# Optimization experiments

Measured on AMD Instinct MI355X. Metric: run time of the kernel, lower is better.

The kernel has to match this reference:

```python
import jax, jax.numpy as jnp
import numpy as np

N_NODES = 10000
N_EDGES = 320000
D = 128      # node/edge feature dim
H = 512      # MLP hidden width


def _mlp(x, W1, b1, W2, b2):
    return jax.nn.relu(x @ W1 + b1) @ W2 + b2


def setup_inputs() -> dict:
    key = jax.random.key(0)
    ks = jax.random.split(key, 8)
    s = lambda fan_in: 1.0 / np.sqrt(fan_in)
    return {
        "x": jax.random.normal(ks[0], (N_NODES, D), jnp.float32),
        "edge_index": jax.random.randint(ks[1], (2, N_EDGES), 0, N_NODES, jnp.int64),
        "edge_attr": jax.random.normal(ks[2], (N_EDGES, D), jnp.float32),
        "We1": jax.random.normal(ks[3], (3 * D, H), jnp.float32) * s(3 * D),
        "be1": jnp.zeros((H,), jnp.float32),
        "We2": jax.random.normal(ks[4], (H, D), jnp.float32) * s(H),
        "be2": jnp.zeros((D,), jnp.float32),
        "Wn1": jax.random.normal(ks[5], (2 * D, H), jnp.float32) * s(2 * D),
        "bn1": jnp.zeros((H,), jnp.float32),
        "Wn2": jax.random.normal(ks[6], (H, D), jnp.float32) * s(H),
        "bn2": jnp.zeros((D,), jnp.float32),
    }


def reference(x, edge_index, edge_attr, We1, be1, We2, be2, Wn1, bn1, Wn2, bn2):
    senders = edge_index[0]
    receivers = edge_index[1]
    # gather -> edge MLP
    edge_inputs = jnp.concatenate([x[senders], x[receivers], edge_attr], axis=-1)  # [E, 3D]
    updated_edge_attr = _mlp(edge_inputs, We1, be1, We2, be2)                      # [E, D]
    # scatter-add into receiving nodes
    aggregated = jax.ops.segment_sum(updated_edge_attr, receivers, num_segments=x.shape[0])  # [N, D]
    # node MLP
    node_inputs = jnp.concatenate([x, aggregated], axis=-1)                        # [N, 2D]
    updated_nodes = _mlp(node_inputs, Wn1, bn1, Wn2, bn2)                          # [N, D]
    return updated_nodes, updated_edge_attr
```

## Files before the change

### kernel.cpp

```cpp
#include <hip/hip_runtime.h>
#include <hip/hip_bf16.h>

#define N_NODES 10000
#define N_EDGES 320000
#define D 128
#define H 512

typedef __bf16 bf16x8 __attribute__((ext_vector_type(8)));
typedef float f32x4 __attribute__((ext_vector_type(4)));
typedef unsigned short u16x8 __attribute__((ext_vector_type(8)));

__device__ __forceinline__ unsigned short f2bf(float f) {
    union { float f; unsigned u; } v; v.f = f;
    unsigned r = v.u + 0x7fffu + ((v.u >> 16) & 1u);
    return (unsigned short)(r >> 16);
}

__global__ void cast_x_kernel(const float* __restrict__ x, unsigned short* __restrict__ xb) {
    int t = blockIdx.x * 256 + threadIdx.x;
    float4 v = reinterpret_cast<const float4*>(x)[t];
    ushort4 o;
    o.x = f2bf(v.x); o.y = f2bf(v.y); o.z = f2bf(v.z); o.w = f2bf(v.w);
    reinterpret_cast<ushort4*>(xb)[t] = o;
}

__global__ void swizzle_w_kernel(const float* __restrict__ W, unsigned short* __restrict__ out,
                                 int K, int Nn) {
    int t = blockIdx.x * 256 + threadIdx.x;
    int total = (K >> 5) * (Nn >> 4) * 64;
    if (t >= total) return;
    int lane = t & 63;
    int tile = t >> 6;
    int ntiles = Nn >> 4;
    int nt = tile % ntiles;
    int kt = tile / ntiles;
    int k0 = kt * 32 + (lane >> 4) * 8;
    int n  = nt * 16 + (lane & 15);
    unsigned short tmp[8];
#pragma unroll
    for (int j = 0; j < 8; ++j) tmp[j] = f2bf(W[(size_t)(k0 + j) * Nn + n]);
    ushort4* dst = reinterpret_cast<ushort4*>(out + (size_t)t * 8);
    dst[0] = *reinterpret_cast<ushort4*>(&tmp[0]);
    dst[1] = *reinterpret_cast<ushort4*>(&tmp[4]);
}

__global__ void hist_kernel(const int* __restrict__ eidx, int* __restrict__ deg) {
    int e = blockIdx.x * 256 + threadIdx.x;
    if (e < N_EDGES) atomicAdd(&deg[eidx[N_EDGES + e]], 1);
}

__global__ __launch_bounds__(1024) void scan_kernel(const int* __restrict__ deg,
                                                    int* __restrict__ rowstart,
                                                    int* __restrict__ cursor) {
    __shared__ int wsums[16];
    const int t = threadIdx.x;
    const int lane = t & 63, wv = t >> 6;
    const int base = t * 10;
    int loc[10];
    int s = 0;
#pragma unroll
    for (int i = 0; i < 10; ++i) {
        int v = (base + i < N_NODES) ? deg[base + i] : 0;
        loc[i] = s; s += v;
    }
    const int tot = s;
    int inc = tot;
#pragma unroll
    for (int d = 1; d < 64; d <<= 1) {
        int n = __shfl_up(inc, d, 64);
        if (lane >= d) inc += n;
    }
    if (lane == 63) wsums[wv] = inc;
    __syncthreads();
    if (t == 0) {
        int run = 0;
#pragma unroll
        for (int w = 0; w < 16; ++w) { int v = wsums[w]; wsums[w] = run; run += v; }
    }
    __syncthreads();
    const int off = wsums[wv] + inc - tot;
#pragma unroll
    for (int i = 0; i < 10; ++i) {
        int idx = base + i;
        if (idx < N_NODES) { int v = off + loc[i]; rowstart[idx] = v; cursor[idx] = v; }
    }
    if (t == 1023) rowstart[N_NODES] = off + tot;
}

__global__ void scatter_kernel(const int* __restrict__ eidx, int* __restrict__ cursor,
                               int* __restrict__ elist) {
    int e = blockIdx.x * 256 + threadIdx.x;
    if (e < N_EDGES) {
        int p = atomicAdd(&cursor[eidx[N_EDGES + e]], 1);
        elist[p] = e;
    }
}

__global__ __launch_bounds__(256) void agg_kernel(
    const float* __restrict__ out_edges,
    const int* __restrict__ rowstart,
    const int* __restrict__ elist,
    unsigned short* __restrict__ aggb)
{
    int node = blockIdx.x * 4 + (threadIdx.x >> 6);
    int lane = threadIdx.x & 63;
    int r0 = rowstart[node], r1 = rowstart[node + 1];
    float sx = 0.f, sy = 0.f;
    for (int j = r0; j < r1; ++j) {
        int e = elist[j];
        float2 v = *reinterpret_cast<const float2*>(&out_edges[(size_t)e * 128 + lane * 2]);
        sx += v.x; sy += v.y;
    }
    ushort2 o; o.x = f2bf(sx); o.y = f2bf(sy);
    *reinterpret_cast<ushort2*>(&aggb[(size_t)node * 128 + lane * 2]) = o;
}

__device__ __forceinline__ void gld_lds16(const void* g, void* l) {
    __builtin_amdgcn_global_load_lds((const __attribute__((address_space(1))) void*)g,
                                     (__attribute__((address_space(3))) void*)l, 16, 0, 0);
}

__device__ __forceinline__ void stage_a(int kt, unsigned short* Abuf, int wave, int lane,
                                        const unsigned short* aS, const unsigned short* aR,
                                        const float* aE) {
    if (kt < 8) {
        const unsigned short* src = (kt < 4) ? (aS + kt * 32) : (aR + (kt - 4) * 32);
        gld_lds16(src, Abuf + wave * 512);
    } else {
        const float* s = aE + (kt - 8) * 32;
        float4 v0 = *reinterpret_cast<const float4*>(s);
        float4 v1 = *reinterpret_cast<const float4*>(s + 4);
        u16x8 o;
        o[0] = f2bf(v0.x); o[1] = f2bf(v0.y); o[2] = f2bf(v0.z); o[3] = f2bf(v0.w);
        o[4] = f2bf(v1.x); o[5] = f2bf(v1.y); o[6] = f2bf(v1.z); o[7] = f2bf(v1.w);
        *reinterpret_cast<u16x8*>(Abuf + wave * 512 + lane * 8) = o;
    }
}

__device__ __forceinline__ void stage_b(int kt, unsigned short* Bbuf, int wave, int lane,
                                        const unsigned short* We1s) {
#pragma unroll
    for (int i = 0; i < 4; ++i) {
        int c = wave * 4 + i;
        const unsigned short* src = We1s + ((size_t)kt * 32 + c) * 512 + lane * 8;
        gld_lds16(src, Bbuf + c * 512);
    }
}

__global__ __launch_bounds__(512, 2) void edge_mlp_kernel(
    const unsigned short* __restrict__ xb,
    const int* __restrict__ eidx,
    const float* __restrict__ edge_attr,
    const unsigned short* __restrict__ We1s,
    const float* __restrict__ be1,
    const unsigned short* __restrict__ We2s,
    const float* __restrict__ be2,
    float* __restrict__ out_edges)
{
    __shared__ unsigned short smem[40960];
    unsigned short* const A0  = smem;
    unsigned short* const A1  = smem + 4096;
    unsigned short* const B0  = smem + 8192;
    unsigned short* const B1  = smem + 24576;
    unsigned short* const sH0 = smem + 4096;
    unsigned short* const sH1 = smem + 21504;

    const int tid = threadIdx.x;
    const int wave = tid >> 6, lane = tid & 63;
    const int wr = wave >> 2, wc = wave & 3;
    const int l15 = lane & 15;
    const int Q = lane >> 4;
    const int e0 = blockIdx.x * 128;

    const int rs = wave * 16 + (lane >> 2);
    const int sq = (lane & 3) ^ (rs & 3);
    const int nS = eidx[e0 + rs];
    const int nR = eidx[N_EDGES + e0 + rs];
    const unsigned short* aS = xb + (size_t)nS * 128 + sq * 8;
    const unsigned short* aR = xb + (size_t)nR * 128 + sq * 8;
    const float*          aE = edge_attr + (size_t)(e0 + rs) * 128 + sq * 8;

    f32x4 acc1[8][4];
#pragma unroll
    for (int j = 0; j < 8; ++j)
#pragma unroll
        for (int mt = 0; mt < 4; ++mt) acc1[j][mt] = (f32x4){0.f, 0.f, 0.f, 0.f};
    f32x4 acc2[2][4];
#pragma unroll
    for (int nn = 0; nn < 2; ++nn)
#pragma unroll
        for (int mt = 0; mt < 4; ++mt) acc2[nn][mt] = (f32x4){0.f, 0.f, 0.f, 0.f};

    stage_a(0, A0, wave, lane, aS, aR, aE);
    stage_b(0, B0, wave, lane, We1s);
    __syncthreads();

#pragma unroll
    for (int kt = 0; kt < 12; ++kt) {
        unsigned short* const Ac = (kt & 1) ? A1 : A0;
        unsigned short* const Bc = (kt & 1) ? B1 : B0;
        if (kt < 11) {
            stage_a(kt + 1, (kt & 1) ? A0 : A1, wave, lane, aS, aR, aE);
            stage_b(kt + 1, (kt & 1) ? B0 : B1, wave, lane, We1s);
        }
        bf16x8 a[4];
#pragma unroll
        for (int mt = 0; mt < 4; ++mt) {
            int R = wr * 64 + mt * 16 + l15;
            a[mt] = *reinterpret_cast<const bf16x8*>(&Ac[R * 32 + ((Q ^ (R & 3)) * 8)]);
        }
#pragma unroll
        for (int j = 0; j < 8; ++j) {
            int ntile = (j >> 1) * 8 + wc * 2 + (j & 1);
            bf16x8 b = *reinterpret_cast<const bf16x8*>(&Bc[ntile * 512 + lane * 8]);
#pragma unroll
            for (int mt = 0; mt < 4; ++mt)
                acc1[j][mt] = __builtin_amdgcn_mfma_f32_16x16x32_bf16(a[mt], b, acc1[j][mt], 0, 0, 0);
        }
        __syncthreads();
    }

#define EWRITE_H(hh, dst)                                                     \
    {                                                                         \
        _Pragma("unroll")                                                     \
        for (int nn = 0; nn < 2; ++nn) {                                      \
            int cc = (wc * 2 + nn) * 16 + l15;                                \
            float bias = be1[(hh) * 128 + cc];                                \
            _Pragma("unroll")                                                 \
            for (int mt = 0; mt < 4; ++mt)                                    \
                _Pragma("unroll")                                             \
                for (int r = 0; r < 4; ++r) {                                 \
                    float v = acc1[(hh) * 2 + nn][mt][r] + bias;              \
                    v = v > 0.f ? v : 0.f;                                    \
                    int row = wr * 64 + mt * 16 + (lane >> 4) * 4 + r;        \
                    (dst)[row * 136 + cc] = f2bf(v);                          \
                }                                                             \
        }                                                                     \
    }

    EWRITE_H(0, sH0);
    __syncthreads();
#pragma unroll
    for (int h = 0; h < 4; ++h) {
        unsigned short* const cur = (h & 1) ? sH1 : sH0;
        unsigned short* const nxt = (h & 1) ? sH0 : sH1;
        if (h < 3) EWRITE_H(h + 1, nxt);
#pragma unroll
        for (int kt = 0; kt < 4; ++kt) {
            bf16x8 a[4];
#pragma unroll
            for (int mt = 0; mt < 4; ++mt) {
                int R = wr * 64 + mt * 16 + l15;
                a[mt] = *reinterpret_cast<const bf16x8*>(&cur[R * 136 + kt * 32 + Q * 8]);
            }
#pragma unroll
            for (int nn = 0; nn < 2; ++nn) {
                int ntile = wc * 2 + nn;
                bf16x8 b = *reinterpret_cast<const bf16x8*>(
                    &We2s[(((size_t)(h * 4 + kt) * 8 + ntile) * 64 + lane) * 8]);
#pragma unroll
                for (int mt = 0; mt < 4; ++mt)
                    acc2[nn][mt] = __builtin_amdgcn_mfma_f32_16x16x32_bf16(a[mt], b, acc2[nn][mt], 0, 0, 0);
            }
        }
        if (h < 3) __syncthreads();
    }

#pragma unroll
    for (int nn = 0; nn < 2; ++nn) {
        int cc = (wc * 2 + nn) * 16 + l15;
        float bias = be2[cc];
#pragma unroll
        for (int mt = 0; mt < 4; ++mt)
#pragma unroll
            for (int r = 0; r < 4; ++r) {
                int row = wr * 64 + mt * 16 + (lane >> 4) * 4 + r;
                __builtin_nontemporal_store(acc2[nn][mt][r] + bias,
                                            &out_edges[(size_t)(e0 + row) * 128 + cc]);
            }
    }
}

#define WRITE_H(hh, dst, B1)                                                  \
    {                                                                         \
        _Pragma("unroll")                                                     \
        for (int nn = 0; nn < 2; ++nn) {                                      \
            int cc = (wave * 2 + nn) * 16 + l15;                              \
            float bias = (B1)[(hh) * 128 + cc];                               \
            _Pragma("unroll")                                                 \
            for (int mt = 0; mt < 4; ++mt)                                    \
                _Pragma("unroll")                                             \
                for (int r = 0; r < 4; ++r) {                                 \
                    float v = acc1[(hh) * 2 + nn][mt][r] + bias;              \
                    v = v > 0.f ? v : 0.f;                                    \
                    int row = mt * 16 + (lane >> 4) * 4 + r;                  \
                    (dst)[row * 136 + cc] = f2bf(v);                          \
                }                                                             \
        }                                                                     \
    }

#define GEMM2_CHUNK(hh, src, W2)                                              \
    {                                                                         \
        _Pragma("unroll")                                                     \
        for (int kt = 0; kt < 4; ++kt) {                                      \
            bf16x8 a[4];                                                      \
            _Pragma("unroll")                                                 \
            for (int mt = 0; mt < 4; ++mt)                                    \
                a[mt] = *reinterpret_cast<const bf16x8*>(                     \
                    &(src)[(mt * 16 + l15) * 136 + kt * 32 + q8]);            \
            _Pragma("unroll")                                                 \
            for (int nn = 0; nn < 2; ++nn) {                                  \
                int ntile = wave * 2 + nn;                                    \
                bf16x8 b = *reinterpret_cast<const bf16x8*>(                  \
                    &(W2)[(((size_t)((hh) * 4 + kt) * 8 + ntile) * 64 + lane) * 8]); \
                _Pragma("unroll")                                             \
                for (int mt = 0; mt < 4; ++mt)                                \
                    acc2[nn][mt] = __builtin_amdgcn_mfma_f32_16x16x32_bf16(   \
                        a[mt], b, acc2[nn][mt], 0, 0, 0);                     \
            }                                                                 \
        }                                                                     \
    }

__global__ __launch_bounds__(256, 2) void node_mlp_kernel(
    const unsigned short* __restrict__ xb,
    const unsigned short* __restrict__ aggb,
    const unsigned short* __restrict__ Wn1s,
    const float* __restrict__ bn1,
    const unsigned short* __restrict__ Wn2s,
    const float* __restrict__ bn2,
    float* __restrict__ out_nodes)
{
    __shared__ unsigned short sA[17408];
    unsigned short* const sH0 = sA;
    unsigned short* const sH1 = sA + 64 * 136;

    const int tid = threadIdx.x;
    const int wave = tid >> 6, lane = tid & 63;
    const int n0 = blockIdx.x * 64;
    const int l15 = lane & 15;
    const int q8 = (lane >> 4) * 8;

    for (int c = tid; c < 1024; c += 256) {
        int row = c >> 4;
        int off = (c & 15) << 3;
        int node = n0 + row;
        bf16x8 v = {};
        if (node < N_NODES)
            v = *reinterpret_cast<const bf16x8*>(&xb[(size_t)node * 128 + off]);
        *reinterpret_cast<bf16x8*>(&sA[row * 264 + off]) = v;
    }
    for (int c = tid; c < 1024; c += 256) {
        int row = c >> 4;
        int off = (c & 15) << 3;
        int node = n0 + row;
        bf16x8 v = {};
        if (node < N_NODES)
            v = *reinterpret_cast<const bf16x8*>(&aggb[(size_t)node * 128 + off]);
        *reinterpret_cast<bf16x8*>(&sA[row * 264 + 128 + off]) = v;
    }
    __syncthreads();

    f32x4 acc1[8][4];
#pragma unroll
    for (int j = 0; j < 8; ++j)
#pragma unroll
        for (int mt = 0; mt < 4; ++mt) acc1[j][mt] = (f32x4){0.f, 0.f, 0.f, 0.f};
    f32x4 acc2[2][4];
#pragma unroll
    for (int nn = 0; nn < 2; ++nn)
#pragma unroll
        for (int mt = 0; mt < 4; ++mt) acc2[nn][mt] = (f32x4){0.f, 0.f, 0.f, 0.f};

#pragma unroll 2
    for (int kt = 0; kt < 8; ++kt) {
        bf16x8 a[4];
#pragma unroll
        for (int mt = 0; mt < 4; ++mt)
            a[mt] = *reinterpret_cast<const bf16x8*>(&sA[(mt * 16 + l15) * 264 + kt * 32 + q8]);
#pragma unroll
        for (int j = 0; j < 8; ++j) {
            int ntile = (j >> 1) * 8 + wave * 2 + (j & 1);
            bf16x8 b = *reinterpret_cast<const bf16x8*>(
                &Wn1s[(((size_t)kt * 32 + ntile) * 64 + lane) * 8]);
#pragma unroll
            for (int mt = 0; mt < 4; ++mt)
                acc1[j][mt] = __builtin_amdgcn_mfma_f32_16x16x32_bf16(a[mt], b, acc1[j][mt], 0, 0, 0);
        }
    }

    __syncthreads();
    WRITE_H(0, sH0, bn1);
    __syncthreads();
#pragma unroll
    for (int h = 0; h < 4; ++h) {
        unsigned short* const cur = (h & 1) ? sH1 : sH0;
        unsigned short* const nxt = (h & 1) ? sH0 : sH1;
        if (h < 3) WRITE_H(h + 1, nxt, bn1);
        GEMM2_CHUNK(h, cur, Wn2s);
        if (h < 3) __syncthreads();
    }

#pragma unroll
    for (int nn = 0; nn < 2; ++nn) {
        int cc = (wave * 2 + nn) * 16 + l15;
        float bias = bn2[cc];
#pragma unroll
        for (int mt = 0; mt < 4; ++mt)
#pragma unroll
            for (int r = 0; r < 4; ++r) {
                int row = mt * 16 + (lane >> 4) * 4 + r;
                int node = n0 + row;
                if (node < N_NODES)
                    out_nodes[(size_t)node * 128 + cc] = acc2[nn][mt][r] + bias;
            }
    }
}

extern "C" void kernel_launch(void* const* d_in, const int* in_sizes, int n_in,
                              void* d_out, int out_size, void* d_ws, size_t ws_size,
                              hipStream_t stream) {
    const float* x         = (const float*)d_in[0];
    const int*   eidx      = (const int*)d_in[1];
    const float* edge_attr = (const float*)d_in[2];
    const float* We1       = (const float*)d_in[3];
    const float* be1       = (const float*)d_in[4];
    const float* We2       = (const float*)d_in[5];
    const float* be2       = (const float*)d_in[6];
    const float* Wn1       = (const float*)d_in[7];
    const float* bn1       = (const float*)d_in[8];
    const float* Wn2       = (const float*)d_in[9];
    const float* bn2       = (const float*)d_in[10];
    float* out = (float*)d_out;

    char* ws = (char*)d_ws;
    size_t off = 0;
    auto alloc = [&](size_t bytes) {
        void* p = ws + off;
        off += (bytes + 255) & ~(size_t)255;
        return p;
    };
    unsigned short* xb   = (unsigned short*)alloc((size_t)N_NODES * D * 2);
    unsigned short* We1s = (unsigned short*)alloc((size_t)384 * 512 * 2);
    unsigned short* We2s = (unsigned short*)alloc((size_t)512 * 128 * 2);
    unsigned short* Wn1s = (unsigned short*)alloc((size_t)256 * 512 * 2);
    unsigned short* Wn2s = (unsigned short*)alloc((size_t)512 * 128 * 2);
    unsigned short* aggb = (unsigned short*)alloc((size_t)N_NODES * D * 2);
    int* deg      = (int*)alloc((size_t)(N_NODES + 1) * 4);
    int* rowstart = (int*)alloc((size_t)(N_NODES + 1) * 4);
    int* cursor   = (int*)alloc((size_t)(N_NODES + 1) * 4);
    int* elist    = (int*)alloc((size_t)N_EDGES * 4);

    float* out_edges = out + (size_t)N_NODES * D;

    hipMemsetAsync(deg, 0, (size_t)N_NODES * sizeof(int), stream);
    cast_x_kernel<<<(N_NODES * D / 4 + 255) / 256, 256, 0, stream>>>(x, xb);
    swizzle_w_kernel<<<(12 * 32 * 64 + 255) / 256, 256, 0, stream>>>(We1, We1s, 384, 512);
    swizzle_w_kernel<<<(16 * 8 * 64 + 255) / 256, 256, 0, stream>>>(We2, We2s, 512, 128);
    swizzle_w_kernel<<<(8 * 32 * 64 + 255) / 256, 256, 0, stream>>>(Wn1, Wn1s, 256, 512);
    swizzle_w_kernel<<<(16 * 8 * 64 + 255) / 256, 256, 0, stream>>>(Wn2, Wn2s, 512, 128);

    hist_kernel<<<(N_EDGES + 255) / 256, 256, 0, stream>>>(eidx, deg);
    scan_kernel<<<1, 1024, 0, stream>>>(deg, rowstart, cursor);
    scatter_kernel<<<(N_EDGES + 255) / 256, 256, 0, stream>>>(eidx, cursor, elist);

    edge_mlp_kernel<<<N_EDGES / 128, 512, 0, stream>>>(
        xb, eidx, edge_attr, We1s, be1, We2s, be2, out_edges);
    agg_kernel<<<N_NODES / 4, 256, 0, stream>>>(out_edges, rowstart, elist, aggb);
    node_mlp_kernel<<<(N_NODES + 63) / 64, 256, 0, stream>>>(
        xb, aggb, Wn1s, bn1, Wn2s, bn2, out);
}
```

Measured before the change: 611.1 us.

## Triple-buffer edge MLP first-layer staging with explicit vmcnt waits

```diff
diff --git a/kernel.cpp b/kernel.cpp
--- a/kernel.cpp
+++ b/kernel.cpp
@@ -106,7 +106,17 @@
     int lane = threadIdx.x & 63;
     int r0 = rowstart[node], r1 = rowstart[node + 1];
     float sx = 0.f, sy = 0.f;
-    for (int j = r0; j < r1; ++j) {
+    int j = r0;
+    for (; j + 4 <= r1; j += 4) {
+        int ea_ = elist[j], eb_ = elist[j + 1], ec_ = elist[j + 2], ed_ = elist[j + 3];
+        float2 va = *reinterpret_cast<const float2*>(&out_edges[(size_t)ea_ * 128 + lane * 2]);
+        float2 vb = *reinterpret_cast<const float2*>(&out_edges[(size_t)eb_ * 128 + lane * 2]);
+        float2 vc = *reinterpret_cast<const float2*>(&out_edges[(size_t)ec_ * 128 + lane * 2]);
+        float2 vd = *reinterpret_cast<const float2*>(&out_edges[(size_t)ed_ * 128 + lane * 2]);
+        sx += (va.x + vb.x) + (vc.x + vd.x);
+        sy += (va.y + vb.y) + (vc.y + vd.y);
+    }
+    for (; j < r1; ++j) {
         int e = elist[j];
         float2 v = *reinterpret_cast<const float2*>(&out_edges[(size_t)e * 128 + lane * 2]);
         sx += v.x; sy += v.y;
@@ -120,32 +130,10 @@
                                      (__attribute__((address_space(3))) void*)l, 16, 0, 0);
 }
 
-__device__ __forceinline__ void stage_a(int kt, unsigned short* Abuf, int wave, int lane,
-                                        const unsigned short* aS, const unsigned short* aR,
-                                        const float* aE) {
-    if (kt < 8) {
-        const unsigned short* src = (kt < 4) ? (aS + kt * 32) : (aR + (kt - 4) * 32);
-        gld_lds16(src, Abuf + wave * 512);
-    } else {
-        const float* s = aE + (kt - 8) * 32;
-        float4 v0 = *reinterpret_cast<const float4*>(s);
-        float4 v1 = *reinterpret_cast<const float4*>(s + 4);
-        u16x8 o;
-        o[0] = f2bf(v0.x); o[1] = f2bf(v0.y); o[2] = f2bf(v0.z); o[3] = f2bf(v0.w);
-        o[4] = f2bf(v1.x); o[5] = f2bf(v1.y); o[6] = f2bf(v1.z); o[7] = f2bf(v1.w);
-        *reinterpret_cast<u16x8*>(Abuf + wave * 512 + lane * 8) = o;
-    }
-}
-
-__device__ __forceinline__ void stage_b(int kt, unsigned short* Bbuf, int wave, int lane,
-                                        const unsigned short* We1s) {
-#pragma unroll
-    for (int i = 0; i < 4; ++i) {
-        int c = wave * 4 + i;
-        const unsigned short* src = We1s + ((size_t)kt * 32 + c) * 512 + lane * 8;
-        gld_lds16(src, Bbuf + c * 512);
-    }
-}
+#define WAITVML(N) do { asm volatile("s_waitcnt vmcnt(" #N ") lgkmcnt(0)" ::: "memory"); \
+                        __builtin_amdgcn_sched_barrier(0); } while (0)
+#define RBAR()     do { __builtin_amdgcn_s_barrier(); \
+                        __builtin_amdgcn_sched_barrier(0); } while (0)
 
 __global__ __launch_bounds__(512, 2) void edge_mlp_kernel(
     const unsigned short* __restrict__ xb,
@@ -157,13 +145,9 @@
     const float* __restrict__ be2,
     float* __restrict__ out_edges)
 {
-    __shared__ unsigned short smem[40960];
-    unsigned short* const A0  = smem;
-    unsigned short* const A1  = smem + 4096;
-    unsigned short* const B0  = smem + 8192;
-    unsigned short* const B1  = smem + 24576;
-    unsigned short* const sH0 = smem + 4096;
-    unsigned short* const sH1 = smem + 21504;
+    __shared__ unsigned short smem[61440];
+    unsigned short* const sH0 = smem;
+    unsigned short* const sH1 = smem + 17408;
 
     const int tid = threadIdx.x;
     const int wave = tid >> 6, lane = tid & 63;
@@ -178,47 +162,80 @@
     const int nR = eidx[N_EDGES + e0 + rs];
     const unsigned short* aS = xb + (size_t)nS * 128 + sq * 8;
     const unsigned short* aR = xb + (size_t)nR * 128 + sq * 8;
-    const float*          aE = edge_attr + (size_t)(e0 + rs) * 128 + sq * 8;
+
+    u16x8 eaw[4];
+    {
+        const float* aE = edge_attr + (size_t)(e0 + rs) * 128 + sq * 8;
+#pragma unroll
+        for (int s = 0; s < 4; ++s) {
+            float4 v0 = *reinterpret_cast<const float4*>(aE + s * 32);
+            float4 v1 = *reinterpret_cast<const float4*>(aE + s * 32 + 4);
+            eaw[s][0] = f2bf(v0.x); eaw[s][1] = f2bf(v0.y);
+            eaw[s][2] = f2bf(v0.z); eaw[s][3] = f2bf(v0.w);
+            eaw[s][4] = f2bf(v1.x); eaw[s][5] = f2bf(v1.y);
+            eaw[s][6] = f2bf(v1.z); eaw[s][7] = f2bf(v1.w);
+        }
+    }
 
     f32x4 acc1[8][4];
 #pragma unroll
     for (int j = 0; j < 8; ++j)
 #pragma unroll
         for (int mt = 0; mt < 4; ++mt) acc1[j][mt] = (f32x4){0.f, 0.f, 0.f, 0.f};
+
+#define STAGE(S) do {                                                                   \
+        if ((S) < 8) {                                                                  \
+            const unsigned short* asrc =                                                \
+                ((S) < 4) ? (aS + (S) * 32) : (aR + ((S) - 4) * 32);                    \
+            gld_lds16(asrc, smem + ((S) % 3) * 4096 + wave * 512);                      \
+        } else {                                                                        \
+            *reinterpret_cast<u16x8*>(&smem[((S) % 3) * 4096 + rs * 32 + (lane & 3) * 8]) \
+                = eaw[(S) - 8];                                                         \
+        }                                                                               \
+        _Pragma("unroll")                                                               \
+        for (int i = 0; i < 4; ++i)                                                     \
+            gld_lds16(We1s + (size_t)(S) * 16384 + (size_t)(wave * 4 + i) * 512 + lane * 8, \
+                      smem + 12288 + ((S) % 3) * 16384 + (wave * 4 + i) * 512);         \
+    } while (0)
+
+#define MF(KT) do {                                                                     \
+        unsigned short* const Ac = smem + ((KT) % 3) * 4096;                            \
+        unsigned short* const Bc = smem + 12288 + ((KT) % 3) * 16384;                   \
+        bf16x8 a[4];                                                                    \
+        _Pragma("unroll")                                                               \
+        for (int mt = 0; mt < 4; ++mt) {                                                \
+            int R = wr * 64 + mt * 16 + l15;                                            \
+            a[mt] = *reinterpret_cast<const bf16x8*>(&Ac[R * 32 + ((Q ^ (R & 3)) * 8)]); \
+        }                                                                               \
+        _Pragma("unroll")                                                               \
+        for (int j = 0; j < 8; ++j) {                                                   \
+            int ntile = (j >> 1) * 8 + wc * 2 + (j & 1);                                \
+            bf16x8 b = *reinterpret_cast<const bf16x8*>(&Bc[ntile * 512 + lane * 8]);   \
+            _Pragma("unroll")                                                           \
+            for (int mt = 0; mt < 4; ++mt)                                              \
+                acc1[j][mt] = __builtin_amdgcn_mfma_f32_16x16x32_bf16(a[mt], b, acc1[j][mt], 0, 0, 0); \
+        }                                                                               \
+    } while (0)
+
+    STAGE(0); STAGE(1);
+    WAITVML(5); RBAR(); STAGE(2);  MF(0);
+    WAITVML(5); RBAR(); STAGE(3);  MF(1);
+    WAITVML(5); RBAR(); STAGE(4);  MF(2);
+    WAITVML(5); RBAR(); STAGE(5);  MF(3);
+    WAITVML(5); RBAR(); STAGE(6);  MF(4);
+    WAITVML(5); RBAR(); STAGE(7);  MF(5);
+    WAITVML(5); RBAR(); STAGE(8);  MF(6);
+    WAITVML(4); RBAR(); STAGE(9);  MF(7);
+    WAITVML(4); RBAR(); STAGE(10); MF(8);
+    WAITVML(4); RBAR(); STAGE(11); MF(9);
+    WAITVML(4); RBAR();            MF(10);
+    WAITVML(0); RBAR();            MF(11);
+
     f32x4 acc2[2][4];
 #pragma unroll
     for (int nn = 0; nn < 2; ++nn)
 #pragma unroll
         for (int mt = 0; mt < 4; ++mt) acc2[nn][mt] = (f32x4){0.f, 0.f, 0.f, 0.f};
-
-    stage_a(0, A0, wave, lane, aS, aR, aE);
-    stage_b(0, B0, wave, lane, We1s);
-    __syncthreads();
-
-#pragma unroll
-    for (int kt = 0; kt < 12; ++kt) {
-        unsigned short* const Ac = (kt & 1) ? A1 : A0;
-        unsigned short* const Bc = (kt & 1) ? B1 : B0;
-        if (kt < 11) {
-            stage_a(kt + 1, (kt & 1) ? A0 : A1, wave, lane, aS, aR, aE);
-            stage_b(kt + 1, (kt & 1) ? B0 : B1, wave, lane, We1s);
-        }
-        bf16x8 a[4];
-#pragma unroll
-        for (int mt = 0; mt < 4; ++mt) {
-            int R = wr * 64 + mt * 16 + l15;
-            a[mt] = *reinterpret_cast<const bf16x8*>(&Ac[R * 32 + ((Q ^ (R & 3)) * 8)]);
-        }
-#pragma unroll
-        for (int j = 0; j < 8; ++j) {
-            int ntile = (j >> 1) * 8 + wc * 2 + (j & 1);
-            bf16x8 b = *reinterpret_cast<const bf16x8*>(&Bc[ntile * 512 + lane * 8]);
-#pragma unroll
-            for (int mt = 0; mt < 4; ++mt)
-                acc1[j][mt] = __builtin_amdgcn_mfma_f32_16x16x32_bf16(a[mt], b, acc1[j][mt], 0, 0, 0);
-        }
-        __syncthreads();
-    }
 
 #define EWRITE_H(hh, dst)                                                     \
     {                                                                         \
@@ -238,6 +255,7 @@
         }                                                                     \
     }
 
+    __syncthreads();
     EWRITE_H(0, sH0);
     __syncthreads();
 #pragma unroll
@@ -275,8 +293,7 @@
 #pragma unroll
             for (int r = 0; r < 4; ++r) {
                 int row = wr * 64 + mt * 16 + (lane >> 4) * 4 + r;
-                __builtin_nontemporal_store(acc2[nn][mt][r] + bias,
-                                            &out_edges[(size_t)(e0 + row) * 128 + cc]);
+                out_edges[(size_t)(e0 + row) * 128 + cc] = acc2[nn][mt][r] + bias;
             }
     }
 }
```

Measured after the change: 594.5 us. 2.7% less time.
